# Optimization experiments

Hardware: AMD Instinct MI355X
Metric: run time of the kernel (lower is better)

Reference implementation:

```python
import jax, jax.numpy as jnp
import numpy as np

D = 256; DFF = 1024; NH = 8; NL = 4; NP_ = 4; HD = D // NH
SHAPES = [(128, 128), (64, 64), (32, 32), (16, 16)]
LEN_IN = sum(h * w for h, w in SHAPES)  # 21760
B = 4; LQ = 1024


def _ln(x, g, b, eps=1e-5):
    m = x.mean(-1, keepdims=True)
    v = ((x - m) ** 2).mean(-1, keepdims=True)
    return (x - m) * jax.lax.rsqrt(v + eps) * g + b


def _ms_core(value, shapes, loc, aw):
    # value (B,Len,NH,HD); loc (B,LQ,NH,NL,NP,2) in [0,1]; aw (B,LQ,NH,NL,NP)
    Bn, Lq = loc.shape[0], loc.shape[1]
    acc = jnp.zeros((Bn, Lq, NH, HD), value.dtype)
    start = 0
    for lvl, (H, W) in enumerate(shapes):
        v = value[:, start:start + H * W]  # (B,HW,NH,HD)
        start += H * W
        l = loc[:, :, :, lvl]  # (B,LQ,NH,NP,2)
        # grid_sample(align_corners=False): pixel = loc*size - 0.5, zero padding
        x = l[..., 0] * W - 0.5
        y = l[..., 1] * H - 0.5
        x0 = jnp.floor(x); y0 = jnp.floor(y)
        fx = x - x0; fy = y - y0
        x0i = x0.astype(jnp.int32); y0i = y0.astype(jnp.int32)
        lvl_out = jnp.zeros((Bn, Lq, NP_, NH, HD), value.dtype)
        for dx, dy, w in ((0, 0, (1 - fx) * (1 - fy)), (1, 0, fx * (1 - fy)),
                          (0, 1, (1 - fx) * fy), (1, 1, fx * fy)):
            xi = x0i + dx; yi = y0i + dy
            ok = ((xi >= 0) & (xi < W) & (yi >= 0) & (yi < H)).astype(value.dtype)
            idx = jnp.clip(yi, 0, H - 1) * W + jnp.clip(xi, 0, W - 1)  # (B,LQ,NH,NP)
            idxf = idx.transpose(0, 1, 3, 2).reshape(Bn, Lq * NP_, NH)
            g = jnp.take_along_axis(v, idxf[..., None], axis=1).reshape(Bn, Lq, NP_, NH, HD)
            lvl_out = lvl_out + g * (w * ok).transpose(0, 1, 3, 2)[..., None]
        awl = aw[:, :, :, lvl].transpose(0, 1, 3, 2)  # (B,LQ,NP,NH)
        acc = acc + (lvl_out * awl[..., None]).sum(axis=2)
    return acc.reshape(Bn, Lq, NH * HD)


def _msda(q, ref, src, shapes, ow, ob, aww, awb, vw, vb, pw, pb):
    Bn, Lq, _ = q.shape
    val = (src @ vw + vb).reshape(Bn, -1, NH, HD)
    off = (q @ ow + ob).reshape(Bn, Lq, NH, NL, NP_, 2)
    aw = jax.nn.softmax((q @ aww + awb).reshape(Bn, Lq, NH, NL * NP_), axis=-1)
    aw = aw.reshape(Bn, Lq, NH, NL, NP_)
    norm = jnp.array([[w_, h_] for h_, w_ in shapes], dtype=q.dtype)  # (L,2)=(W,H)
    loc = ref[:, :, None, :, None, :] + off / norm[None, None, None, :, None, :]
    return _ms_core(val, shapes, loc, aw) @ pw + pb


def setup_inputs():
    key = jax.random.key(0)
    ks = iter(jax.random.split(key, 48))
    def n(shape, s=1.0):
        return jax.random.normal(next(ks), shape, jnp.float32) * s
    inp = {
        "tgt": n((B, LQ, D)),
        "query_pos": n((B, LQ, D)),
        "reference_points": jax.random.uniform(next(ks), (B, LQ, NL, 2), jnp.float32),
        "src_rgb": n((B, LEN_IN, D)),
        "src_thermal": n((B, LEN_IN, D)),
    }
    for p in ("rgb", "th"):
        inp[p + "_off_w"] = n((D, NH * NL * NP_ * 2), 0.02)
        inp[p + "_off_b"] = n((NH * NL * NP_ * 2,), 0.02)
        inp[p + "_aw_w"] = n((D, NH * NL * NP_), 0.02)
        inp[p + "_aw_b"] = n((NH * NL * NP_,), 0.02)
        inp[p + "_val_w"] = n((D, D), 0.02); inp[p + "_val_b"] = jnp.zeros((D,))
        inp[p + "_out_w"] = n((D, D), 0.02); inp[p + "_out_b"] = jnp.zeros((D,))
    inp["ln_rgb_g"] = jnp.ones((D,)); inp["ln_rgb_b"] = jnp.zeros((D,))
    inp["ln_th_g"] = jnp.ones((D,)); inp["ln_th_b"] = jnp.zeros((D,))
    inp["ffn_w1"] = n((D, DFF), 0.02); inp["ffn_b1"] = jnp.zeros((DFF,))
    inp["ffn_w2"] = n((DFF, D), 0.02); inp["ffn_b2"] = jnp.zeros((D,))
    inp["ln2_g"] = jnp.ones((D,)); inp["ln2_b"] = jnp.zeros((D,))
    inp["spatial_shapes"] = jnp.array(SHAPES, dtype=jnp.int32)
    return inp


def reference(tgt, query_pos, reference_points, src_rgb, src_thermal,
              rgb_off_w, rgb_off_b, rgb_aw_w, rgb_aw_b, rgb_val_w, rgb_val_b, rgb_out_w, rgb_out_b,
              th_off_w, th_off_b, th_aw_w, th_aw_b, th_val_w, th_val_b, th_out_w, th_out_b,
              ln_rgb_g, ln_rgb_b, ln_th_g, ln_th_b,
              ffn_w1, ffn_b1, ffn_w2, ffn_b2, ln2_g, ln2_b,
              spatial_shapes):
    shapes = [(int(h), int(w)) for h, w in np.asarray(spatial_shapes)]
    q = tgt + query_pos
    t_rgb = _msda(q, reference_points, src_rgb, shapes,
                  rgb_off_w, rgb_off_b, rgb_aw_w, rgb_aw_b,
                  rgb_val_w, rgb_val_b, rgb_out_w, rgb_out_b)
    tgt_rgb = _ln(tgt + t_rgb, ln_rgb_g, ln_rgb_b)
    # thermal branch: computed by the source module but discarded (tgt_fused = tgt_rgb)
    t_th = _msda(q, reference_points, src_thermal, shapes,
                 th_off_w, th_off_b, th_aw_w, th_aw_b,
                 th_val_w, th_val_b, th_out_w, th_out_b)
    _ = _ln(tgt + t_th, ln_th_g, ln_th_b)
    fused = tgt_rgb
    t2 = jnp.maximum(fused @ ffn_w1 + ffn_b1, 0.0) @ ffn_w2 + ffn_b2
    return _ln(fused + t2, ln2_g, ln2_b)
```

## Files before the change

kernel.cpp:

```cpp
#include <hip/hip_runtime.h>

typedef __bf16 v8bf __attribute__((ext_vector_type(8)));
typedef float  v4f  __attribute__((ext_vector_type(4)));

#define D_     256
#define NH_    8
#define NL_    4
#define NP2_   4
#define HD_    32
#define BB_    4
#define LQ_    1024
#define LEN_IN_ 21760
#define BQ_    4096
#define DFF_   1024

template<bool A_BF16, bool RELU, bool OUT_BF16>
__global__ __launch_bounds__(256) void gemm_tn(
    const void* __restrict__ Av, const __bf16* __restrict__ Bt,
    const float* __restrict__ bias, void* __restrict__ Cv,
    int M, int N, int K, int lda, int ldc)
{
    __shared__ alignas(16) __bf16 As[128][72];
    __shared__ alignas(16) __bf16 Bs[128][72];

    const int tid  = threadIdx.x;
    const int row0 = blockIdx.y * 128;
    const int col0 = blockIdx.x * 128;
    const int lane = tid & 63;
    const int wid  = tid >> 6;
    const int wm   = (wid >> 1) * 64;
    const int wn   = (wid & 1) * 64;
    const int lr   = lane & 15;
    const int lk   = lane >> 4;

    v4f acc[4][4];
    #pragma unroll
    for (int i = 0; i < 4; ++i)
        #pragma unroll
        for (int j = 0; j < 4; ++j) {
            acc[i][j][0] = 0.f; acc[i][j][1] = 0.f;
            acc[i][j][2] = 0.f; acc[i][j][3] = 0.f;
        }

    const int nkt = K >> 6;
    for (int kt = 0; kt < nkt; ++kt) {
        const int k0 = kt << 6;
        __syncthreads();
        #pragma unroll
        for (int i = 0; i < 4; ++i) {
            const int c  = tid + i * 256;
            const int r  = c >> 3;
            const int cc = c & 7;
            if constexpr (A_BF16) {
                const __bf16* A = (const __bf16*)Av;
                const uint4 u = *(const uint4*)(A + (size_t)(row0 + r) * lda + k0 + cc * 8);
                *(uint4*)(&As[r][cc * 8]) = u;
            } else {
                const float* A = (const float*)Av;
                const float* p = A + (size_t)(row0 + r) * lda + k0 + cc * 8;
                const float4 f0 = *(const float4*)p;
                const float4 f1 = *(const float4*)(p + 4);
                v8bf t;
                t[0] = (__bf16)f0.x; t[1] = (__bf16)f0.y;
                t[2] = (__bf16)f0.z; t[3] = (__bf16)f0.w;
                t[4] = (__bf16)f1.x; t[5] = (__bf16)f1.y;
                t[6] = (__bf16)f1.z; t[7] = (__bf16)f1.w;
                *(v8bf*)(&As[r][cc * 8]) = t;
            }
            const uint4 ub = *(const uint4*)(Bt + (size_t)(col0 + r) * K + k0 + cc * 8);
            *(uint4*)(&Bs[r][cc * 8]) = ub;
        }
        __syncthreads();
        #pragma unroll
        for (int kk = 0; kk < 2; ++kk) {
            v8bf a[4], b[4];
            #pragma unroll
            for (int i = 0; i < 4; ++i)
                a[i] = *(const v8bf*)(&As[wm + i * 16 + lr][kk * 32 + lk * 8]);
            #pragma unroll
            for (int j = 0; j < 4; ++j)
                b[j] = *(const v8bf*)(&Bs[wn + j * 16 + lr][kk * 32 + lk * 8]);
            #pragma unroll
            for (int i = 0; i < 4; ++i)
                #pragma unroll
                for (int j = 0; j < 4; ++j)
                    acc[i][j] = __builtin_amdgcn_mfma_f32_16x16x32_bf16(a[i], b[j], acc[i][j], 0, 0, 0);
        }
    }

    float bv[4];
    #pragma unroll
    for (int j = 0; j < 4; ++j) bv[j] = bias[col0 + wn + j * 16 + lr];

    #pragma unroll
    for (int i = 0; i < 4; ++i) {
        #pragma unroll
        for (int j = 0; j < 4; ++j) {
            const int col = col0 + wn + j * 16 + lr;
            #pragma unroll
            for (int r = 0; r < 4; ++r) {
                const int row = row0 + wm + i * 16 + lk * 4 + r;
                float v = acc[i][j][r] + bv[j];
                if constexpr (RELU) v = fmaxf(v, 0.f);
                if constexpr (OUT_BF16)
                    ((__bf16*)Cv)[(size_t)row * ldc + col] = (__bf16)v;
                else
                    ((float*)Cv)[(size_t)row * ldc + col] = v;
            }
        }
    }
}

__global__ void transpose_cvt(const float* __restrict__ in, __bf16* __restrict__ out,
                              int K, int N)
{
    const int idx = blockIdx.x * 256 + threadIdx.x;
    if (idx >= K * N) return;
    const int n = idx / K;
    const int k = idx - n * K;
    out[idx] = (__bf16)in[(size_t)k * N + n];
}

__global__ void bias_cat(const float* __restrict__ a, const float* __restrict__ b,
                         float* __restrict__ out)
{
    const int i = threadIdx.x;
    out[i] = (i < 256) ? a[i] : b[i - 256];
}

__global__ void add4(const float* __restrict__ a, const float* __restrict__ b,
                     float* __restrict__ o)
{
    const int i = blockIdx.x * 256 + threadIdx.x;
    const float4 x = ((const float4*)a)[i];
    const float4 y = ((const float4*)b)[i];
    float4 r; r.x = x.x + y.x; r.y = x.y + y.y; r.z = x.z + y.z; r.w = x.w + y.w;
    ((float4*)o)[i] = r;
}

__global__ __launch_bounds__(256) void samp_prep(
    const float* __restrict__ offaw,
    const float* __restrict__ refp,
    float* __restrict__ samp)
{
    const int t  = blockIdx.x * 256 + threadIdx.x;
    const int bq = t >> 3;
    const int h  = t & 7;
    const float* base = offaw + (size_t)bq * 384;
    const float* awp  = base + 256 + h * 16;

    float e[16];
    float m = -1e30f;
    #pragma unroll
    for (int j = 0; j < 16; ++j) m = fmaxf(m, awp[j]);
    float s = 0.f;
    #pragma unroll
    for (int j = 0; j < 16; ++j) { e[j] = __expf(awp[j] - m); s += e[j]; }
    const float inv = 1.f / s;

    const float SZ[4] = {128.f, 64.f, 32.f, 16.f};
    float* sp = samp + (size_t)t * 48;
    #pragma unroll
    for (int l = 0; l < 4; ++l) {
        const float rx = refp[(size_t)bq * 8 + l * 2 + 0];
        const float ry = refp[(size_t)bq * 8 + l * 2 + 1];
        const float W = SZ[l], H = SZ[l];
        #pragma unroll
        for (int p = 0; p < 4; ++p) {
            const float ox = base[h * 32 + l * 8 + p * 2 + 0];
            const float oy = base[h * 32 + l * 8 + p * 2 + 1];
            const float locx = rx + ox * (1.f / W);
            const float locy = ry + oy * (1.f / H);
            sp[(l * 4 + p) * 3 + 0] = locx * W - 0.5f;
            sp[(l * 4 + p) * 3 + 1] = locy * H - 0.5f;
            sp[(l * 4 + p) * 3 + 2] = e[l * 4 + p] * inv;
        }
    }
}

__global__ __launch_bounds__(256) void ms_sample(
    const __bf16* __restrict__ val,
    const float* __restrict__ samp,
    float* __restrict__ out)
{
    const int g    = blockIdx.x * 8 + (threadIdx.x >> 5);
    const int lane = threadIdx.x & 31;
    const int bq   = g >> 3;
    const int h    = g & 7;
    const int b    = bq >> 10;

    const int   Wi[4] = {128, 64, 32, 16};
    const int   st[4] = {0, 16384, 20480, 21504};
    const float* sp = samp + (size_t)g * 48;
    const __bf16* vb = val + (size_t)b * LEN_IN_ * 256 + h * 32 + lane;

    float acc = 0.f;
    #pragma unroll
    for (int l = 0; l < 4; ++l) {
        const int W = Wi[l], H = Wi[l];
        const __bf16* vl = vb + (size_t)st[l] * 256;
        #pragma unroll
        for (int p = 0; p < 4; ++p) {
            const float x  = sp[(l * 4 + p) * 3 + 0];
            const float y  = sp[(l * 4 + p) * 3 + 1];
            const float aw = sp[(l * 4 + p) * 3 + 2];
            const float xf = floorf(x), yf = floorf(y);
            const float fx = x - xf, fy = y - yf;
            const int x0 = (int)xf, y0 = (int)yf;
            const float w00 = (1.f - fx) * (1.f - fy) * aw;
            const float w10 = fx * (1.f - fy) * aw;
            const float w01 = (1.f - fx) * fy * aw;
            const float w11 = fx * fy * aw;
            const bool xi0 = (x0 >= 0) & (x0 < W);
            const bool xi1 = (x0 + 1 >= 0) & (x0 + 1 < W);
            const bool yi0 = (y0 >= 0) & (y0 < H);
            const bool yi1 = (y0 + 1 >= 0) & (y0 + 1 < H);
            if (xi0 & yi0) acc += w00 * (float)vl[(size_t)(y0 * W + x0) * 256];
            if (xi1 & yi0) acc += w10 * (float)vl[(size_t)(y0 * W + x0 + 1) * 256];
            if (xi0 & yi1) acc += w01 * (float)vl[(size_t)((y0 + 1) * W + x0) * 256];
            if (xi1 & yi1) acc += w11 * (float)vl[(size_t)((y0 + 1) * W + x0 + 1) * 256];
        }
    }
    out[(size_t)bq * 256 + h * 32 + lane] = acc;
}

__global__ __launch_bounds__(256) void ln_residual(
    const float* __restrict__ a, const float* __restrict__ d,
    const float* __restrict__ g, const float* __restrict__ be,
    float* __restrict__ out)
{
    const int row  = blockIdx.x * 4 + (threadIdx.x >> 6);
    const int lane = threadIdx.x & 63;
    const size_t base = (size_t)row * 256 + lane * 4;
    const float4 av = *(const float4*)(a + base);
    const float4 dv = *(const float4*)(d + base);
    float x0 = av.x + dv.x, x1 = av.y + dv.y, x2 = av.z + dv.z, x3 = av.w + dv.w;
    float s  = x0 + x1 + x2 + x3;
    float sq = x0 * x0 + x1 * x1 + x2 * x2 + x3 * x3;
    #pragma unroll
    for (int m = 1; m < 64; m <<= 1) {
        s  += __shfl_xor(s, m);
        sq += __shfl_xor(sq, m);
    }
    const float mean = s * (1.f / 256.f);
    const float var  = sq * (1.f / 256.f) - mean * mean;
    const float inv  = rsqrtf(var + 1e-5f);
    const float4 gv = *(const float4*)(g + lane * 4);
    const float4 bv = *(const float4*)(be + lane * 4);
    float4 r;
    r.x = (x0 - mean) * inv * gv.x + bv.x;
    r.y = (x1 - mean) * inv * gv.y + bv.y;
    r.z = (x2 - mean) * inv * gv.z + bv.z;
    r.w = (x3 - mean) * inv * gv.w + bv.w;
    *(float4*)(out + base) = r;
}

extern "C" void kernel_launch(void* const* d_in, const int* in_sizes, int n_in,
                              void* d_out, int out_size, void* d_ws, size_t ws_size,
                              hipStream_t stream)
{
    const float* tgt    = (const float*)d_in[0];
    const float* qpos   = (const float*)d_in[1];
    const float* refp   = (const float*)d_in[2];
    const float* src    = (const float*)d_in[3];
    const float* off_w  = (const float*)d_in[5];
    const float* off_b  = (const float*)d_in[6];
    const float* aw_w   = (const float*)d_in[7];
    const float* aw_b   = (const float*)d_in[8];
    const float* val_w  = (const float*)d_in[9];
    const float* val_b  = (const float*)d_in[10];
    const float* out_w  = (const float*)d_in[11];
    const float* out_b  = (const float*)d_in[12];
    const float* ln_g   = (const float*)d_in[21];
    const float* ln_b   = (const float*)d_in[22];
    const float* w1     = (const float*)d_in[25];
    const float* b1     = (const float*)d_in[26];
    const float* w2     = (const float*)d_in[27];
    const float* b2     = (const float*)d_in[28];
    const float* ln2_g  = (const float*)d_in[29];
    const float* ln2_b  = (const float*)d_in[30];
    float* out = (float*)d_out;

    char* ws = (char*)d_ws;
    size_t woff = 0;
    auto alloc = [&](size_t bytes) { char* p = ws + woff; woff += (bytes + 255) & ~(size_t)255; return p; };

    __bf16* vwt     = (__bf16*)alloc(256 * 256 * 2);
    __bf16* offawt  = (__bf16*)alloc(384 * 256 * 2);
    __bf16* pwt     = (__bf16*)alloc(256 * 256 * 2);
    __bf16* w1t     = (__bf16*)alloc(1024 * 256 * 2);
    __bf16* w2t     = (__bf16*)alloc(256 * 1024 * 2);
    float*  biascat = (float*)alloc(384 * 4);
    float*  qbuf    = (float*)alloc((size_t)BQ_ * 256 * 4);
    __bf16* valb    = (__bf16*)alloc((size_t)BB_ * LEN_IN_ * 256 * 2);
    float*  offaw   = (float*)alloc((size_t)BQ_ * 384 * 4);
    float*  samp    = (float*)alloc((size_t)BQ_ * NH_ * 48 * 4);
    float*  sacc    = (float*)alloc((size_t)BQ_ * 256 * 4);
    float*  tproj   = (float*)alloc((size_t)BQ_ * 256 * 4);
    float*  tgtrgb  = (float*)alloc((size_t)BQ_ * 256 * 4);
    __bf16* hbuf    = (__bf16*)alloc((size_t)BQ_ * 1024 * 2);
    float*  t2      = (float*)alloc((size_t)BQ_ * 256 * 4);
    (void)ws_size; (void)in_sizes; (void)n_in; (void)out_size;

    transpose_cvt<<<dim3(256), 256, 0, stream>>>(val_w, vwt, 256, 256);
    transpose_cvt<<<dim3(256), 256, 0, stream>>>(off_w, offawt, 256, 256);
    transpose_cvt<<<dim3(128), 256, 0, stream>>>(aw_w, offawt + 256 * 256, 256, 128);
    transpose_cvt<<<dim3(256), 256, 0, stream>>>(out_w, pwt, 256, 256);
    transpose_cvt<<<dim3(1024), 256, 0, stream>>>(w1, w1t, 256, 1024);
    transpose_cvt<<<dim3(1024), 256, 0, stream>>>(w2, w2t, 1024, 256);
    bias_cat<<<1, 384, 0, stream>>>(off_b, aw_b, biascat);
    add4<<<dim3(1024), 256, 0, stream>>>(tgt, qpos, qbuf);

    gemm_tn<false, false, true><<<dim3(2, 680), 256, 0, stream>>>(
        src, vwt, val_b, valb, BB_ * LEN_IN_, 256, 256, 256, 256);

    gemm_tn<false, false, false><<<dim3(3, 32), 256, 0, stream>>>(
        qbuf, offawt, biascat, offaw, BQ_, 384, 256, 256, 384);

    samp_prep<<<dim3(128), 256, 0, stream>>>(offaw, refp, samp);

    ms_sample<<<dim3(4096), 256, 0, stream>>>(valb, samp, sacc);

    gemm_tn<false, false, false><<<dim3(2, 32), 256, 0, stream>>>(
        sacc, pwt, out_b, tproj, BQ_, 256, 256, 256, 256);

    ln_residual<<<dim3(1024), 256, 0, stream>>>(tgt, tproj, ln_g, ln_b, tgtrgb);

    gemm_tn<false, true, true><<<dim3(8, 32), 256, 0, stream>>>(
        tgtrgb, w1t, b1, hbuf, BQ_, 1024, 256, 256, 1024);
    gemm_tn<true, false, false><<<dim3(2, 32), 256, 0, stream>>>(
        hbuf, w2t, b2, t2, BQ_, 256, 1024, 1024, 256);

    ln_residual<<<dim3(1024), 256, 0, stream>>>(tgtrgb, t2, ln2_g, ln2_b, out);
}
```

Before: 384.5 us.

## Stream value projection with resident weights, fuse query add, merge transposes, smaller GEMM tiles

Replaces the value-projection GEMM with a persistent kernel that keeps the whole 256x256 bf16 weight in LDS (pre-swizzled) and streams 16-row chunks of src per wave. The six weight transposes become one tiled LDS transpose kernel. The tgt+query_pos add is fused into the offset/attention GEMM's A load. The small M=4096 GEMMs move to 64-row tiles to give more blocks. The sampler uses clamped unconditional loads with mask weights instead of branches. This trades some register and LDS pressure for fewer launches and less redundant weight traffic in the dominant value GEMM.

```diff
diff --git a/kernel.cpp b/kernel.cpp
--- a/kernel.cpp
+++ b/kernel.cpp
@@ -3,26 +3,126 @@
 typedef __bf16 v8bf __attribute__((ext_vector_type(8)));
 typedef float  v4f  __attribute__((ext_vector_type(4)));
 
-#define D_     256
-#define NH_    8
-#define NL_    4
-#define NP2_   4
-#define HD_    32
 #define BB_    4
 #define LQ_    1024
 #define LEN_IN_ 21760
 #define BQ_    4096
-#define DFF_   1024
-
-template<bool A_BF16, bool RELU, bool OUT_BF16>
+#define MV_    87040
+#define NCHUNK_ 5440
+#define NWAVES_ 2048
+
+__global__ __launch_bounds__(256) void transpose_all(
+    const float* __restrict__ off_w, const float* __restrict__ aw_w,
+    const float* __restrict__ out_w, const float* __restrict__ w1,
+    const float* __restrict__ w2,    const float* __restrict__ val_w,
+    __bf16* __restrict__ offawt, __bf16* __restrict__ pwt,
+    __bf16* __restrict__ w1t,    __bf16* __restrict__ w2t,
+    __bf16* __restrict__ vwt_sw)
+{
+    const int b = blockIdx.x;
+    if (b >= 672) {
+        const int g = b - 672;
+        const int n = threadIdx.x;
+        v8bf t;
+        #pragma unroll
+        for (int e = 0; e < 8; ++e)
+            t[e] = (__bf16)val_w[(size_t)(g * 8 + e) * 256 + n];
+        *(v8bf*)(vwt_sw + (size_t)g * 2048 + n * 8) = t;
+        return;
+    }
+    const float* in; __bf16* out; int K, N, tileid;
+    if (b < 64)       { in = off_w; out = offawt;            K = 256;  N = 256;  tileid = b; }
+    else if (b < 96)  { in = aw_w;  out = offawt + 256*256;  K = 256;  N = 128;  tileid = b - 64; }
+    else if (b < 160) { in = out_w; out = pwt;               K = 256;  N = 256;  tileid = b - 96; }
+    else if (b < 416) { in = w1;    out = w1t;               K = 256;  N = 1024; tileid = b - 160; }
+    else              { in = w2;    out = w2t;               K = 1024; N = 256;  tileid = b - 416; }
+    const int ntn = N >> 5;
+    const int k0 = (tileid / ntn) * 32;
+    const int n0 = (tileid % ntn) * 32;
+    __shared__ float ts[32][33];
+    const int r = threadIdx.x >> 5, c = threadIdx.x & 31;
+    #pragma unroll
+    for (int i = 0; i < 4; ++i)
+        ts[r + i * 8][c] = in[(size_t)(k0 + r + i * 8) * N + n0 + c];
+    __syncthreads();
+    #pragma unroll
+    for (int i = 0; i < 4; ++i)
+        out[(size_t)(n0 + r + i * 8) * K + k0 + c] = (__bf16)ts[c][r + i * 8];
+}
+
+__global__ void bias_cat(const float* __restrict__ a, const float* __restrict__ b,
+                         float* __restrict__ out)
+{
+    const int i = threadIdx.x;
+    out[i] = (i < 256) ? a[i] : b[i - 256];
+}
+
+__global__ __launch_bounds__(512, 1) void val_stream(
+    const float* __restrict__ A, const __bf16* __restrict__ Bsw,
+    const float* __restrict__ bias, __bf16* __restrict__ C)
+{
+    __shared__ __bf16 Bs[65536];
+    const int tid = threadIdx.x;
+    #pragma unroll
+    for (int i = 0; i < 16; ++i) {
+        const int cc = tid + i * 512;
+        *(uint4*)(Bs + cc * 8) = *(const uint4*)(Bsw + cc * 8);
+    }
+    __syncthreads();
+
+    const int wid  = tid >> 6, lane = tid & 63;
+    const int lr   = lane & 15;
+    const int lk   = lane >> 4;
+    const int w    = blockIdx.x * 8 + wid;
+
+    float bv[16];
+    #pragma unroll
+    for (int j = 0; j < 16; ++j) bv[j] = bias[j * 16 + lr];
+
+    for (int c = w; c < NCHUNK_; c += NWAVES_) {
+        const float* ap = A + (size_t)(c * 16 + lr) * 256 + lk * 8;
+        float4 a[16];
+        #pragma unroll
+        for (int s = 0; s < 8; ++s) {
+            a[2 * s]     = *(const float4*)(ap + s * 32);
+            a[2 * s + 1] = *(const float4*)(ap + s * 32 + 4);
+        }
+        v4f acc[16];
+        #pragma unroll
+        for (int j = 0; j < 16; ++j) {
+            acc[j][0] = 0.f; acc[j][1] = 0.f; acc[j][2] = 0.f; acc[j][3] = 0.f;
+        }
+        #pragma unroll
+        for (int s = 0; s < 8; ++s) {
+            v8bf af;
+            af[0] = (__bf16)a[2*s].x;   af[1] = (__bf16)a[2*s].y;
+            af[2] = (__bf16)a[2*s].z;   af[3] = (__bf16)a[2*s].w;
+            af[4] = (__bf16)a[2*s+1].x; af[5] = (__bf16)a[2*s+1].y;
+            af[6] = (__bf16)a[2*s+1].z; af[7] = (__bf16)a[2*s+1].w;
+            const __bf16* bp = Bs + (s * 4 + lk) * 2048 + lr * 8;
+            #pragma unroll
+            for (int j = 0; j < 16; ++j) {
+                const v8bf bf_ = *(const v8bf*)(bp + j * 128);
+                acc[j] = __builtin_amdgcn_mfma_f32_16x16x32_bf16(af, bf_, acc[j], 0, 0, 0);
+            }
+        }
+        __bf16* cp = C + (size_t)(c * 16 + lk * 4) * 256 + lr;
+        #pragma unroll
+        for (int j = 0; j < 16; ++j)
+            #pragma unroll
+            for (int r = 0; r < 4; ++r)
+                cp[r * 256 + j * 16] = (__bf16)(acc[j][r] + bv[j]);
+    }
+}
+
+template<bool RELU, bool OUT_BF16>
 __global__ __launch_bounds__(256) void gemm_tn(
-    const void* __restrict__ Av, const __bf16* __restrict__ Bt,
+    const float* __restrict__ A, const __bf16* __restrict__ Bt,
     const float* __restrict__ bias, void* __restrict__ Cv,
-    int M, int N, int K, int lda, int ldc)
+    int K, int lda, int ldc)
 {
     __shared__ alignas(16) __bf16 As[128][72];
     __shared__ alignas(16) __bf16 Bs[128][72];
-
     const int tid  = threadIdx.x;
     const int row0 = blockIdx.y * 128;
     const int col0 = blockIdx.x * 128;
@@ -38,8 +138,7 @@
     for (int i = 0; i < 4; ++i)
         #pragma unroll
         for (int j = 0; j < 4; ++j) {
-            acc[i][j][0] = 0.f; acc[i][j][1] = 0.f;
-            acc[i][j][2] = 0.f; acc[i][j][3] = 0.f;
+            acc[i][j][0] = 0.f; acc[i][j][1] = 0.f; acc[i][j][2] = 0.f; acc[i][j][3] = 0.f;
         }
 
     const int nkt = K >> 6;
@@ -51,35 +150,23 @@
             const int c  = tid + i * 256;
             const int r  = c >> 3;
             const int cc = c & 7;
-            if constexpr (A_BF16) {
-                const __bf16* A = (const __bf16*)Av;
-                const uint4 u = *(const uint4*)(A + (size_t)(row0 + r) * lda + k0 + cc * 8);
-                *(uint4*)(&As[r][cc * 8]) = u;
-            } else {
-                const float* A = (const float*)Av;
-                const float* p = A + (size_t)(row0 + r) * lda + k0 + cc * 8;
-                const float4 f0 = *(const float4*)p;
-                const float4 f1 = *(const float4*)(p + 4);
-                v8bf t;
-                t[0] = (__bf16)f0.x; t[1] = (__bf16)f0.y;
-                t[2] = (__bf16)f0.z; t[3] = (__bf16)f0.w;
-                t[4] = (__bf16)f1.x; t[5] = (__bf16)f1.y;
-                t[6] = (__bf16)f1.z; t[7] = (__bf16)f1.w;
-                *(v8bf*)(&As[r][cc * 8]) = t;
-            }
-            const uint4 ub = *(const uint4*)(Bt + (size_t)(col0 + r) * K + k0 + cc * 8);
-            *(uint4*)(&Bs[r][cc * 8]) = ub;
+            const float* p = A + (size_t)(row0 + r) * lda + k0 + cc * 8;
+            const float4 f0 = *(const float4*)p;
+            const float4 f1 = *(const float4*)(p + 4);
+            v8bf t;
+            t[0] = (__bf16)f0.x; t[1] = (__bf16)f0.y; t[2] = (__bf16)f0.z; t[3] = (__bf16)f0.w;
+            t[4] = (__bf16)f1.x; t[5] = (__bf16)f1.y; t[6] = (__bf16)f1.z; t[7] = (__bf16)f1.w;
+            *(v8bf*)(&As[r][cc * 8]) = t;
+            *(uint4*)(&Bs[r][cc * 8]) = *(const uint4*)(Bt + (size_t)(col0 + r) * K + k0 + cc * 8);
         }
         __syncthreads();
         #pragma unroll
         for (int kk = 0; kk < 2; ++kk) {
             v8bf a[4], b[4];
             #pragma unroll
-            for (int i = 0; i < 4; ++i)
-                a[i] = *(const v8bf*)(&As[wm + i * 16 + lr][kk * 32 + lk * 8]);
-            #pragma unroll
-            for (int j = 0; j < 4; ++j)
-                b[j] = *(const v8bf*)(&Bs[wn + j * 16 + lr][kk * 32 + lk * 8]);
+            for (int i = 0; i < 4; ++i) a[i] = *(const v8bf*)(&As[wm + i * 16 + lr][kk * 32 + lk * 8]);
+            #pragma unroll
+            for (int j = 0; j < 4; ++j) b[j] = *(const v8bf*)(&Bs[wn + j * 16 + lr][kk * 32 + lk * 8]);
             #pragma unroll
             for (int i = 0; i < 4; ++i)
                 #pragma unroll
@@ -91,9 +178,8 @@
     float bv[4];
     #pragma unroll
     for (int j = 0; j < 4; ++j) bv[j] = bias[col0 + wn + j * 16 + lr];
-
-    #pragma unroll
-    for (int i = 0; i < 4; ++i) {
+    #pragma unroll
+    for (int i = 0; i < 4; ++i)
         #pragma unroll
         for (int j = 0; j < 4; ++j) {
             const int col = col0 + wn + j * 16 + lr;
@@ -102,40 +188,93 @@
                 const int row = row0 + wm + i * 16 + lk * 4 + r;
                 float v = acc[i][j][r] + bv[j];
                 if constexpr (RELU) v = fmaxf(v, 0.f);
-                if constexpr (OUT_BF16)
-                    ((__bf16*)Cv)[(size_t)row * ldc + col] = (__bf16)v;
-                else
-                    ((float*)Cv)[(size_t)row * ldc + col] = v;
+                if constexpr (OUT_BF16) ((__bf16*)Cv)[(size_t)row * ldc + col] = (__bf16)v;
+                else                    ((float*)Cv)[(size_t)row * ldc + col] = v;
             }
         }
-    }
-}
-
-__global__ void transpose_cvt(const float* __restrict__ in, __bf16* __restrict__ out,
-                              int K, int N)
-{
-    const int idx = blockIdx.x * 256 + threadIdx.x;
-    if (idx >= K * N) return;
-    const int n = idx / K;
-    const int k = idx - n * K;
-    out[idx] = (__bf16)in[(size_t)k * N + n];
-}
-
-__global__ void bias_cat(const float* __restrict__ a, const float* __restrict__ b,
-                         float* __restrict__ out)
-{
-    const int i = threadIdx.x;
-    out[i] = (i < 256) ? a[i] : b[i - 256];
-}
-
-__global__ void add4(const float* __restrict__ a, const float* __restrict__ b,
-                     float* __restrict__ o)
-{
-    const int i = blockIdx.x * 256 + threadIdx.x;
-    const float4 x = ((const float4*)a)[i];
-    const float4 y = ((const float4*)b)[i];
-    float4 r; r.x = x.x + y.x; r.y = x.y + y.y; r.z = x.z + y.z; r.w = x.w + y.w;
-    ((float4*)o)[i] = r;
+}
+
+template<int AMODE, bool OUT_BF16>
+__global__ __launch_bounds__(256) void gemm_tn64(
+    const void* __restrict__ Av, const void* __restrict__ A2v,
+    const __bf16* __restrict__ Bt, const float* __restrict__ bias,
+    void* __restrict__ Cv, int K, int lda, int ldc)
+{
+    __shared__ alignas(16) __bf16 As[64][72];
+    __shared__ alignas(16) __bf16 Bs[128][72];
+    const int tid  = threadIdx.x;
+    const int row0 = blockIdx.y * 64;
+    const int col0 = blockIdx.x * 128;
+    const int lane = tid & 63;
+    const int wid  = tid >> 6;
+    const int wm   = wid * 16;
+    const int lr   = lane & 15;
+    const int lk   = lane >> 4;
+
+    v4f acc[8];
+    #pragma unroll
+    for (int j = 0; j < 8; ++j) { acc[j][0]=0.f; acc[j][1]=0.f; acc[j][2]=0.f; acc[j][3]=0.f; }
+
+    const int nkt = K >> 6;
+    for (int kt = 0; kt < nkt; ++kt) {
+        const int k0 = kt << 6;
+        __syncthreads();
+        #pragma unroll
+        for (int i = 0; i < 2; ++i) {
+            const int c  = tid + i * 256;
+            const int r  = c >> 3;
+            const int cc = c & 7;
+            if constexpr (AMODE == 2) {
+                const __bf16* Ab = (const __bf16*)Av;
+                *(uint4*)(&As[r][cc * 8]) = *(const uint4*)(Ab + (size_t)(row0 + r) * lda + k0 + cc * 8);
+            } else {
+                const float* p = (const float*)Av + (size_t)(row0 + r) * lda + k0 + cc * 8;
+                float4 f0 = *(const float4*)p;
+                float4 f1 = *(const float4*)(p + 4);
+                if constexpr (AMODE == 1) {
+                    const float* q = (const float*)A2v + (size_t)(row0 + r) * lda + k0 + cc * 8;
+                    const float4 g0 = *(const float4*)q;
+                    const float4 g1 = *(const float4*)(q + 4);
+                    f0.x += g0.x; f0.y += g0.y; f0.z += g0.z; f0.w += g0.w;
+                    f1.x += g1.x; f1.y += g1.y; f1.z += g1.z; f1.w += g1.w;
+                }
+                v8bf t;
+                t[0] = (__bf16)f0.x; t[1] = (__bf16)f0.y; t[2] = (__bf16)f0.z; t[3] = (__bf16)f0.w;
+                t[4] = (__bf16)f1.x; t[5] = (__bf16)f1.y; t[6] = (__bf16)f1.z; t[7] = (__bf16)f1.w;
+                *(v8bf*)(&As[r][cc * 8]) = t;
+            }
+        }
+        #pragma unroll
+        for (int i = 0; i < 4; ++i) {
+            const int c  = tid + i * 256;
+            const int r  = c >> 3;
+            const int cc = c & 7;
+            *(uint4*)(&Bs[r][cc * 8]) = *(const uint4*)(Bt + (size_t)(col0 + r) * K + k0 + cc * 8);
+        }
+        __syncthreads();
+        #pragma unroll
+        for (int kk = 0; kk < 2; ++kk) {
+            const v8bf a = *(const v8bf*)(&As[wm + lr][kk * 32 + lk * 8]);
+            #pragma unroll
+            for (int j = 0; j < 8; ++j) {
+                const v8bf b = *(const v8bf*)(&Bs[j * 16 + lr][kk * 32 + lk * 8]);
+                acc[j] = __builtin_amdgcn_mfma_f32_16x16x32_bf16(a, b, acc[j], 0, 0, 0);
+            }
+        }
+    }
+
+    #pragma unroll
+    for (int j = 0; j < 8; ++j) {
+        const int col = col0 + j * 16 + lr;
+        const float bvj = bias[col];
+        #pragma unroll
+        for (int r = 0; r < 4; ++r) {
+            const int row = row0 + wm + lk * 4 + r;
+            const float v = acc[j][r] + bvj;
+            if constexpr (OUT_BF16) ((__bf16*)Cv)[(size_t)row * ldc + col] = (__bf16)v;
+            else                    ((float*)Cv)[(size_t)row * ldc + col] = v;
+        }
+    }
 }
 
 __global__ __launch_bounds__(256) void samp_prep(
@@ -164,15 +303,13 @@
     for (int l = 0; l < 4; ++l) {
         const float rx = refp[(size_t)bq * 8 + l * 2 + 0];
         const float ry = refp[(size_t)bq * 8 + l * 2 + 1];
-        const float W = SZ[l], H = SZ[l];
+        const float W = SZ[l];
         #pragma unroll
         for (int p = 0; p < 4; ++p) {
             const float ox = base[h * 32 + l * 8 + p * 2 + 0];
             const float oy = base[h * 32 + l * 8 + p * 2 + 1];
-            const float locx = rx + ox * (1.f / W);
-            const float locy = ry + oy * (1.f / H);
-            sp[(l * 4 + p) * 3 + 0] = locx * W - 0.5f;
-            sp[(l * 4 + p) * 3 + 1] = locy * H - 0.5f;
+            sp[(l * 4 + p) * 3 + 0] = (rx + ox * (1.f / W)) * W - 0.5f;
+            sp[(l * 4 + p) * 3 + 1] = (ry + oy * (1.f / W)) * W - 0.5f;
             sp[(l * 4 + p) * 3 + 2] = e[l * 4 + p] * inv;
         }
     }
@@ -189,15 +326,15 @@
     const int h    = g & 7;
     const int b    = bq >> 10;
 
-    const int   Wi[4] = {128, 64, 32, 16};
-    const int   st[4] = {0, 16384, 20480, 21504};
+    const int Wi[4] = {128, 64, 32, 16};
+    const int st[4] = {0, 16384, 20480, 21504};
     const float* sp = samp + (size_t)g * 48;
     const __bf16* vb = val + (size_t)b * LEN_IN_ * 256 + h * 32 + lane;
 
     float acc = 0.f;
     #pragma unroll
     for (int l = 0; l < 4; ++l) {
-        const int W = Wi[l], H = Wi[l];
+        const int W = Wi[l];
         const __bf16* vl = vb + (size_t)st[l] * 256;
         #pragma unroll
         for (int p = 0; p < 4; ++p) {
@@ -207,18 +344,22 @@
             const float xf = floorf(x), yf = floorf(y);
             const float fx = x - xf, fy = y - yf;
             const int x0 = (int)xf, y0 = (int)yf;
-            const float w00 = (1.f - fx) * (1.f - fy) * aw;
-            const float w10 = fx * (1.f - fy) * aw;
-            const float w01 = (1.f - fx) * fy * aw;
-            const float w11 = fx * fy * aw;
-            const bool xi0 = (x0 >= 0) & (x0 < W);
-            const bool xi1 = (x0 + 1 >= 0) & (x0 + 1 < W);
-            const bool yi0 = (y0 >= 0) & (y0 < H);
-            const bool yi1 = (y0 + 1 >= 0) & (y0 + 1 < H);
-            if (xi0 & yi0) acc += w00 * (float)vl[(size_t)(y0 * W + x0) * 256];
-            if (xi1 & yi0) acc += w10 * (float)vl[(size_t)(y0 * W + x0 + 1) * 256];
-            if (xi0 & yi1) acc += w01 * (float)vl[(size_t)((y0 + 1) * W + x0) * 256];
-            if (xi1 & yi1) acc += w11 * (float)vl[(size_t)((y0 + 1) * W + x0 + 1) * 256];
+            const float okx0 = (x0 >= 0 && x0 < W) ? 1.f : 0.f;
+            const float okx1 = (x0 + 1 >= 0 && x0 + 1 < W) ? 1.f : 0.f;
+            const float oky0 = (y0 >= 0 && y0 < W) ? 1.f : 0.f;
+            const float oky1 = (y0 + 1 >= 0 && y0 + 1 < W) ? 1.f : 0.f;
+            const int x0c = min(max(x0, 0), W - 1);
+            const int x1c = min(max(x0 + 1, 0), W - 1);
+            const int y0c = min(max(y0, 0), W - 1);
+            const int y1c = min(max(y0 + 1, 0), W - 1);
+            const float v00 = (float)vl[(size_t)(y0c * W + x0c) * 256];
+            const float v10 = (float)vl[(size_t)(y0c * W + x1c) * 256];
+            const float v01 = (float)vl[(size_t)(y1c * W + x0c) * 256];
+            const float v11 = (float)vl[(size_t)(y1c * W + x1c) * 256];
+            acc += aw * ((1.f - fx) * (1.f - fy) * okx0 * oky0 * v00
+                       + fx * (1.f - fy) * okx1 * oky0 * v10
+                       + (1.f - fx) * fy * okx0 * oky1 * v01
+                       + fx * fy * okx1 * oky1 * v11);
         }
     }
     out[(size_t)bq * 256 + h * 32 + lane] = acc;
@@ -238,10 +379,7 @@
     float s  = x0 + x1 + x2 + x3;
     float sq = x0 * x0 + x1 * x1 + x2 * x2 + x3 * x3;
     #pragma unroll
-    for (int m = 1; m < 64; m <<= 1) {
-        s  += __shfl_xor(s, m);
-        sq += __shfl_xor(sq, m);
-    }
+    for (int m = 1; m < 64; m <<= 1) { s += __shfl_xor(s, m); sq += __shfl_xor(sq, m); }
     const float mean = s * (1.f / 256.f);
     const float var  = sq * (1.f / 256.f) - mean * mean;
     const float inv  = rsqrtf(var + 1e-5f);
@@ -285,16 +423,15 @@
     size_t woff = 0;
     auto alloc = [&](size_t bytes) { char* p = ws + woff; woff += (bytes + 255) & ~(size_t)255; return p; };
 
-    __bf16* vwt     = (__bf16*)alloc(256 * 256 * 2);
+    __bf16* vwt_sw  = (__bf16*)alloc(256 * 256 * 2);
     __bf16* offawt  = (__bf16*)alloc(384 * 256 * 2);
     __bf16* pwt     = (__bf16*)alloc(256 * 256 * 2);
     __bf16* w1t     = (__bf16*)alloc(1024 * 256 * 2);
     __bf16* w2t     = (__bf16*)alloc(256 * 1024 * 2);
     float*  biascat = (float*)alloc(384 * 4);
-    float*  qbuf    = (float*)alloc((size_t)BQ_ * 256 * 4);
-    __bf16* valb    = (__bf16*)alloc((size_t)BB_ * LEN_IN_ * 256 * 2);
+    __bf16* valb    = (__bf16*)alloc((size_t)MV_ * 256 * 2);
     float*  offaw   = (float*)alloc((size_t)BQ_ * 384 * 4);
-    float*  samp    = (float*)alloc((size_t)BQ_ * NH_ * 48 * 4);
+    float*  samp    = (float*)alloc((size_t)BQ_ * 8 * 48 * 4);
     float*  sacc    = (float*)alloc((size_t)BQ_ * 256 * 4);
     float*  tproj   = (float*)alloc((size_t)BQ_ * 256 * 4);
     float*  tgtrgb  = (float*)alloc((size_t)BQ_ * 256 * 4);
@@ -302,34 +439,27 @@
     float*  t2      = (float*)alloc((size_t)BQ_ * 256 * 4);
     (void)ws_size; (void)in_sizes; (void)n_in; (void)out_size;
 
-    transpose_cvt<<<dim3(256), 256, 0, stream>>>(val_w, vwt, 256, 256);
-    transpose_cvt<<<dim3(256), 256, 0, stream>>>(off_w, offawt, 256, 256);
-    transpose_cvt<<<dim3(128), 256, 0, stream>>>(aw_w, offawt + 256 * 256, 256, 128);
-    transpose_cvt<<<dim3(256), 256, 0, stream>>>(out_w, pwt, 256, 256);
-    transpose_cvt<<<dim3(1024), 256, 0, stream>>>(w1, w1t, 256, 1024);
-    transpose_cvt<<<dim3(1024), 256, 0, stream>>>(w2, w2t, 1024, 256);
+    transpose_all<<<704, 256, 0, stream>>>(off_w, aw_w, out_w, w1, w2, val_w,
+                                           offawt, pwt, w1t, w2t, vwt_sw);
     bias_cat<<<1, 384, 0, stream>>>(off_b, aw_b, biascat);
-    add4<<<dim3(1024), 256, 0, stream>>>(tgt, qpos, qbuf);
-
-    gemm_tn<false, false, true><<<dim3(2, 680), 256, 0, stream>>>(
-        src, vwt, val_b, valb, BB_ * LEN_IN_, 256, 256, 256, 256);
-
-    gemm_tn<false, false, false><<<dim3(3, 32), 256, 0, stream>>>(
-        qbuf, offawt, biascat, offaw, BQ_, 384, 256, 256, 384);
-
-    samp_prep<<<dim3(128), 256, 0, stream>>>(offaw, refp, samp);
-
-    ms_sample<<<dim3(4096), 256, 0, stream>>>(valb, samp, sacc);
-
-    gemm_tn<false, false, false><<<dim3(2, 32), 256, 0, stream>>>(
-        sacc, pwt, out_b, tproj, BQ_, 256, 256, 256, 256);
-
-    ln_residual<<<dim3(1024), 256, 0, stream>>>(tgt, tproj, ln_g, ln_b, tgtrgb);
-
-    gemm_tn<false, true, true><<<dim3(8, 32), 256, 0, stream>>>(
-        tgtrgb, w1t, b1, hbuf, BQ_, 1024, 256, 256, 1024);
-    gemm_tn<true, false, false><<<dim3(2, 32), 256, 0, stream>>>(
-        hbuf, w2t, b2, t2, BQ_, 256, 1024, 1024, 256);
-
-    ln_residual<<<dim3(1024), 256, 0, stream>>>(tgtrgb, t2, ln2_g, ln2_b, out);
-}
+
+    val_stream<<<256, 512, 0, stream>>>(src, vwt_sw, val_b, valb);
+
+    gemm_tn64<1, false><<<dim3(3, 64), 256, 0, stream>>>(
+        tgt, qpos, offawt, biascat, offaw, 256, 256, 384);
+
+    samp_prep<<<128, 256, 0, stream>>>(offaw, refp, samp);
+    ms_sample<<<4096, 256, 0, stream>>>(valb, samp, sacc);
+
+    gemm_tn64<0, false><<<dim3(2, 64), 256, 0, stream>>>(
+        sacc, nullptr, pwt, out_b, tproj, 256, 256, 256);
+
+    ln_residual<<<1024, 256, 0, stream>>>(tgt, tproj, ln_g, ln_b, tgtrgb);
+
+    gemm_tn<true, true><<<dim3(8, 32), 256, 0, stream>>>(
+        tgtrgb, w1t, b1, hbuf, 256, 256, 1024);
+    gemm_tn64<2, false><<<dim3(2, 64), 256, 0, stream>>>(
+        hbuf, nullptr, w2t, b2, t2, 1024, 1024, 256);
+
+    ln_residual<<<1024, 256, 0, stream>>>(tgtrgb, t2, ln2_g, ln2_b, out);
+}
```

Result: slower. 578.4 us (+50.4%).
